# Performance work log

Hardware: AMD Instinct MI355X
Metric: run time of the kernel (lower is better)

The kernel has to match this reference:

```python
import jax, jax.numpy as jnp
import numpy as np

WS = 7       # window size per spatial dim
SHIFT = 3    # cyclic shift = WS // 2
HEADS = 6


def _rel_pos_index():
    # [N, N] index into the (2*WS-1)^3 relative-position-bias table
    c = np.stack(np.meshgrid(np.arange(WS), np.arange(WS), np.arange(WS), indexing='ij')).reshape(3, -1)
    rel = (c[:, :, None] - c[:, None, :]).transpose(1, 2, 0) + (WS - 1)
    rel[:, :, 0] *= (2 * WS - 1) ** 2
    rel[:, :, 1] *= (2 * WS - 1)
    return rel.sum(-1)


def _attn_mask(D, H, W):
    # shifted-window attention mask: [nW, N, N] with 0 / -100
    img = np.zeros((D, H, W))
    sl = (slice(0, -WS), slice(-WS, -SHIFT), slice(-SHIFT, None))
    cnt = 0
    for d in sl:
        for h in sl:
            for w in sl:
                img[d, h, w] = cnt
                cnt += 1
    m = img.reshape(D // WS, WS, H // WS, WS, W // WS, WS).transpose(0, 2, 4, 1, 3, 5).reshape(-1, WS ** 3)
    return np.where(m[:, None, :] != m[:, :, None], -100.0, 0.0).astype(np.float32)


def _ln(x, g, b):
    mu = x.mean(-1, keepdims=True)
    var = ((x - mu) ** 2).mean(-1, keepdims=True)
    return (x - mu) * jax.lax.rsqrt(var + 1e-5) * g + b


def _win_part(x):
    B, D, H, W, C = x.shape
    x = x.reshape(B, D // WS, WS, H // WS, WS, W // WS, WS, C)
    return x.transpose(0, 1, 3, 5, 2, 4, 6, 7).reshape(B, -1, WS ** 3, C)


def _win_rev(xw, D, H, W):
    B, _, _, C = xw.shape
    x = xw.reshape(B, D // WS, H // WS, W // WS, WS, WS, WS, C)
    return x.transpose(0, 1, 4, 2, 5, 3, 6, 7).reshape(B, D, H, W, C)


def setup_inputs() -> dict:
    key = jax.random.key(0)
    ks = jax.random.split(key, 8)
    C, dff, Nh = 192, 768, HEADS
    s = 0.02
    return {
        'x': jax.random.normal(ks[0], (2, 28, 28, 28, C), jnp.float32),
        'ln1_g': jnp.ones((C,), jnp.float32),
        'ln1_b': jnp.zeros((C,), jnp.float32),
        'qkv_w': jax.random.normal(ks[1], (3 * C, C), jnp.float32) * s,
        'qkv_b': jnp.zeros((3 * C,), jnp.float32),
        'rpb': jax.random.normal(ks[2], ((2 * WS - 1) ** 3, Nh), jnp.float32) * s,
        'proj_w': jax.random.normal(ks[3], (C, C), jnp.float32) * s,
        'proj_b': jnp.zeros((C,), jnp.float32),
        'ln2_g': jnp.ones((C,), jnp.float32),
        'ln2_b': jnp.zeros((C,), jnp.float32),
        'fc1_w': jax.random.normal(ks[4], (dff, C), jnp.float32) * s,
        'fc1_b': jnp.zeros((dff,), jnp.float32),
        'fc2_w': jax.random.normal(ks[5], (C, dff), jnp.float32) * s,
        'fc2_b': jnp.zeros((C,), jnp.float32),
    }


def reference(x, ln1_g, ln1_b, qkv_w, qkv_b, rpb, proj_w, proj_b, ln2_g, ln2_b, fc1_w, fc1_b, fc2_w, fc2_b):
    B, D, H, W, C = x.shape
    hd = C // HEADS
    N = WS ** 3
    idx = jnp.asarray(_rel_pos_index())          # [N, N] int
    mask = jnp.asarray(_attn_mask(D, H, W))      # [nW, N, N]

    shortcut = x
    h = _ln(x, ln1_g, ln1_b)
    h = jnp.roll(h, (-SHIFT, -SHIFT, -SHIFT), axis=(1, 2, 3))
    xw = _win_part(h)                            # [B, nW, N, C]
    nW = xw.shape[1]

    qkv = xw @ qkv_w.T + qkv_b                   # [B, nW, N, 3C]
    qkv = qkv.reshape(B, nW, N, 3, HEADS, hd).transpose(3, 0, 1, 4, 2, 5)  # [3,B,nW,h,N,hd]
    q, k, v = qkv[0], qkv[1], qkv[2]

    scale = hd ** -0.5
    attn = jnp.einsum('bwhnd,bwhmd->bwhnm', q * scale, k)  # [B,nW,h,N,N]
    bias = rpb[idx].transpose(2, 0, 1)           # [h, N, N]
    attn = attn + bias + mask[None, :, None]
    attn = jax.nn.softmax(attn, axis=-1)

    o = jnp.einsum('bwhnm,bwhmd->bwhnd', attn, v)
    o = o.transpose(0, 1, 3, 2, 4).reshape(B, nW, N, C)
    o = o @ proj_w.T + proj_b
    o = _win_rev(o, D, H, W)
    o = jnp.roll(o, (SHIFT, SHIFT, SHIFT), axis=(1, 2, 3))

    x = shortcut + o
    h2 = _ln(x, ln2_g, ln2_b)
    h2 = jax.nn.gelu(h2 @ fc1_w.T + fc1_b, approximate=False)
    return x + (h2 @ fc2_w.T + fc2_b)
```

## Files before the change

kernel.cpp:

```cpp
#include <hip/hip_runtime.h>
#include <hip/hip_bf16.h>
#include <math.h>

typedef __hip_bfloat16 bf16;
typedef unsigned short u16;
typedef __attribute__((ext_vector_type(8))) short bf16x8;
typedef __attribute__((ext_vector_type(4))) float f32x4;
typedef __attribute__((ext_vector_type(16))) float f32x16;
typedef __attribute__((ext_vector_type(4))) unsigned u32x4;

__device__ __forceinline__ float us2f(u16 u) { return __uint_as_float(((unsigned)u) << 16); }
__device__ __forceinline__ u16 f2us(float f) { bf16 h = __float2bfloat16(f); return *(u16*)&h; }

__device__ __forceinline__ float wave_bcast_sum(float v) {
#pragma unroll
    for (int off = 32; off > 0; off >>= 1) v += __shfl_down(v, off);
    return __shfl(v, 0);
}

__device__ __forceinline__ void glds16(const u16* g, u16* l) {
    __builtin_amdgcn_global_load_lds((const __attribute__((address_space(1))) void*)g,
                                     (__attribute__((address_space(3))) void*)l, 16, 0, 0);
}

__global__ __launch_bounds__(256) void k_prep(
    const float* __restrict__ qkv_w, const float* __restrict__ proj_w,
    const float* __restrict__ rpb,
    u16* __restrict__ qkv_wb, u16* __restrict__ proj_wb, float* __restrict__ biasF)
{
    int idx = blockIdx.x * 256 + threadIdx.x;
    if (idx < 110592) { qkv_wb[idx] = f2us(qkv_w[idx]); return; }
    idx -= 110592;
    if (idx < 36864) { proj_wb[idx] = f2us(proj_w[idx]); return; }
    idx -= 36864;
    if (idx >= 6 * 11 * 11 * 1024) return;
    int r16 = idx & 15;
    int lane = (idx >> 4) & 63;
    int cell = idx >> 10;
    int chunk = cell % 11;
    int t2 = cell / 11;
    int tile = t2 % 11;
    int h = t2 / 11;
    int g = r16 >> 2, q = r16 & 3;
    int hi = lane >> 5, l31 = lane & 31;
    int n = tile * 32 + l31;
    int m = chunk * 32 + 4 * hi + 8 * g + q;
    float v = 0.0f;
    if (m < 343 && n < 343) {
        int ni = n / 49, nr = n - ni * 49, nj = nr / 7, nk = nr - nj * 7;
        int mi = m / 49, mr = m - mi * 49, mj = mr / 7, mk = mr - mj * 7;
        int d = (ni - mi) * 169 + (nj - mj) * 13 + (nk - mk) + 1098;
        v = rpb[d * 6 + h] * 5.656854249492381f;
    }
    biasF[idx] = v;
}

__global__ __launch_bounds__(256) void k_f2b2(
    const float* __restrict__ fc1_w, const float* __restrict__ fc2_w,
    u16* __restrict__ fc1_wb, u16* __restrict__ fc2_wb)
{
    int idx = blockIdx.x * 256 + threadIdx.x;
    if (idx < 147456) fc1_wb[idx] = f2us(fc1_w[idx]);
    else fc2_wb[idx - 147456] = f2us(fc2_w[idx - 147456]);
}

__global__ __launch_bounds__(256) void k_ln1_winpart(
    const float* __restrict__ x, const float* __restrict__ g, const float* __restrict__ b,
    u16* __restrict__ out)
{
    int lane = threadIdx.x & 63;
    int t = blockIdx.x * 4 + (threadIdx.x >> 6);
    int bidx = t / (64 * 343);
    int r = t - bidx * (64 * 343);
    int w = r / 343;
    int n = r - w * 343;
    int wd = w >> 4, wh = (w >> 2) & 3, ww = w & 3;
    int i = n / 49, rem = n - i * 49;
    int j = rem / 7, k = rem - j * 7;
    int sd = wd * 7 + i + 3; if (sd >= 28) sd -= 28;
    int sh = wh * 7 + j + 3; if (sh >= 28) sh -= 28;
    int sw = ww * 7 + k + 3; if (sw >= 28) sw -= 28;
    size_t src = ((((size_t)bidx * 28 + sd) * 28 + sh) * 28 + sw) * 192;
    float v0 = x[src + lane], v1 = x[src + lane + 64], v2 = x[src + lane + 128];
    float s  = wave_bcast_sum(v0 + v1 + v2);
    float mu = s * (1.0f / 192.0f);
    float s2 = wave_bcast_sum(v0 * v0 + v1 * v1 + v2 * v2);
    float rs = rsqrtf(s2 * (1.0f / 192.0f) - mu * mu + 1e-5f);
    u16* op = out + (size_t)t * 192;
    op[lane]       = f2us((v0 - mu) * rs * g[lane]       + b[lane]);
    op[lane + 64]  = f2us((v1 - mu) * rs * g[lane + 64]  + b[lane + 64]);
    op[lane + 128] = f2us((v2 - mu) * rs * g[lane + 128] + b[lane + 128]);
}

__global__ __launch_bounds__(256) void k_add_winrev_ln2(
    const float* __restrict__ x, const u16* __restrict__ projw,
    const float* __restrict__ g, const float* __restrict__ b,
    float* __restrict__ x1, u16* __restrict__ h2)
{
    int lane = threadIdx.x & 63;
    int t = blockIdx.x * 4 + (threadIdx.x >> 6);
    int sw_ = t % 28, t1 = t / 28;
    int sh_ = t1 % 28, t2 = t1 / 28;
    int sd_ = t2 % 28, bidx = t2 / 28;
    int rd = sd_ + 25; if (rd >= 28) rd -= 28;
    int rh = sh_ + 25; if (rh >= 28) rh -= 28;
    int rw = sw_ + 25; if (rw >= 28) rw -= 28;
    int wd = rd / 7, i = rd - wd * 7;
    int wh = rh / 7, j = rh - wh * 7;
    int ww = rw / 7, k = rw - ww * 7;
    int w = (wd << 4) + (wh << 2) + ww;
    int n = (i * 7 + j) * 7 + k;
    size_t src = (((size_t)(bidx * 64 + w)) * 343 + n) * 192;
    const float* xp = x + (size_t)t * 192;
    float v0 = xp[lane]       + us2f(projw[src + lane]);
    float v1 = xp[lane + 64]  + us2f(projw[src + lane + 64]);
    float v2 = xp[lane + 128] + us2f(projw[src + lane + 128]);
    float* op = x1 + (size_t)t * 192;
    op[lane] = v0; op[lane + 64] = v1; op[lane + 128] = v2;
    float s  = wave_bcast_sum(v0 + v1 + v2);
    float mu = s * (1.0f / 192.0f);
    float s2 = wave_bcast_sum(v0 * v0 + v1 * v1 + v2 * v2);
    float rs = rsqrtf(s2 * (1.0f / 192.0f) - mu * mu + 1e-5f);
    u16* hp = h2 + (size_t)t * 192;
    hp[lane]       = f2us((v0 - mu) * rs * g[lane]       + b[lane]);
    hp[lane + 64]  = f2us((v1 - mu) * rs * g[lane + 64]  + b[lane + 64]);
    hp[lane + 128] = f2us((v2 - mu) * rs * g[lane + 128] + b[lane + 128]);
}

template<int ACT, int OUT, int GX>
__global__ __launch_bounds__(256) void k_gemm_mfma(
    const u16* __restrict__ A, const u16* __restrict__ W, const float* __restrict__ bias,
    u16* __restrict__ outB, float* __restrict__ outF, const float* __restrict__ resid,
    int M, int Nc, int K)
{
    __shared__ __align__(16) u16 As[2][128 * 64];
    __shared__ __align__(16) u16 Bs[2][64 * 64];
    int tid = threadIdx.x;
    int lane = tid & 63, wv = tid >> 6;
    int quad = lane >> 4, l16 = lane & 15;

    int nwg = gridDim.x, orig = blockIdx.x;
    int q = nwg >> 3, r = nwg & 7;
    int xcd = orig & 7, lin = orig >> 3;
    int L = (xcd < r ? xcd * (q + 1) : r * (q + 1) + (xcd - r) * q) + lin;
    int bx = L % GX, by = L / GX;
    int m0 = by << 7, n0 = bx << 6;

    f32x4 acc[2][4] = {};

    int srow = wv * 8 + (lane >> 3);
    int swz  = ((lane & 7) << 3) ^ (((lane >> 3) & 7) << 3);
    const u16* gA = A + (size_t)(m0 + srow) * K + swz;
    const u16* gB = W + (size_t)(n0 + srow) * K + swz;
    int rsA = 32 * K;

    int nst = K >> 6;
#define STAGE(buf, k0)                                                        \
    {                                                                         \
        _Pragma("unroll")                                                     \
        for (int i = 0; i < 4; i++)                                           \
            glds16(gA + (size_t)i * rsA + (k0), &As[buf][(i * 4 + wv) * 512]); \
        _Pragma("unroll")                                                     \
        for (int i = 0; i < 2; i++)                                           \
            glds16(gB + (size_t)i * rsA + (k0), &Bs[buf][(i * 4 + wv) * 512]); \
    }

    STAGE(0, 0);
    asm volatile("s_waitcnt vmcnt(0)" ::: "memory");
    __builtin_amdgcn_s_barrier();

    int rswz = (l16 & 7) << 3;
    int cur = 0;
    for (int t = 0; t < nst; ++t) {
        if (t + 1 < nst) STAGE(cur ^ 1, (t + 1) << 6);
#pragma unroll
        for (int kk = 0; kk < 2; kk++) {
            int ko = (kk * 32 + quad * 8) ^ rswz;
            bf16x8 af[2], bfr[4];
#pragma unroll
            for (int mt = 0; mt < 2; mt++)
                af[mt] = *(const bf16x8*)&As[cur][(wv * 32 + mt * 16 + l16) * 64 + ko];
#pragma unroll
            for (int nt = 0; nt < 4; nt++)
                bfr[nt] = *(const bf16x8*)&Bs[cur][(nt * 16 + l16) * 64 + ko];
#pragma unroll
            for (int mt = 0; mt < 2; mt++)
#pragma unroll
                for (int nt = 0; nt < 4; nt++)
                    acc[mt][nt] = __builtin_amdgcn_mfma_f32_16x16x32_bf16(af[mt], bfr[nt], acc[mt][nt], 0, 0, 0);
        }
        asm volatile("s_waitcnt vmcnt(0)" ::: "memory");
        __builtin_amdgcn_s_barrier();
        cur ^= 1;
    }
#undef STAGE
#pragma unroll
    for (int mt = 0; mt < 2; mt++) {
#pragma unroll
        for (int nt = 0; nt < 4; nt++) {
#pragma unroll
            for (int r2 = 0; r2 < 4; r2++) {
                int m = m0 + wv * 32 + mt * 16 + quad * 4 + r2;
                int n = n0 + nt * 16 + l16;
                float v = acc[mt][nt][r2] + bias[n];
                if (ACT == 1) v = 0.5f * v * (1.0f + erff(v * 0.70710678118654752f));
                size_t off = (size_t)m * Nc + n;
                if (OUT == 1) outB[off] = f2us(v);
                else outF[off] = resid[off] + v;
            }
        }
    }
}

__global__ __launch_bounds__(704, 6) void k_attn(
    const u16* __restrict__ qkv, const float* __restrict__ biasF, u16* __restrict__ o_win)
{
    int head = blockIdx.x;
    int w = blockIdx.y;
    int bidx = blockIdx.z;
    __shared__ __align__(16) u16 Ks[352 * 40];
    __shared__ __align__(16) u16 Vt[32 * 360];
    __shared__ unsigned char lab[352];
    int tid = threadIdx.x;
    int lane = tid & 63, wv = tid >> 6;
    int hi = lane >> 5, l31 = lane & 31;
    size_t base = ((size_t)(bidx * 64 + w)) * 343;

    for (int i = tid; i < 2816; i += 704) {
        int m = i >> 3;
        int d4 = (i & 7) << 2;
        ushort4 kv = {0, 0, 0, 0}, vv = {0, 0, 0, 0};
        if (m < 343) {
            size_t off = (base + m) * 576 + head * 32 + d4;
            kv = *(const ushort4*)(qkv + off + 192);
            vv = *(const ushort4*)(qkv + off + 384);
        }
        *(ushort4*)&Ks[m * 40 + d4] = kv;
        Vt[(d4 + 0) * 360 + m] = vv.x;
        Vt[(d4 + 1) * 360 + m] = vv.y;
        Vt[(d4 + 2) * 360 + m] = vv.z;
        Vt[(d4 + 3) * 360 + m] = vv.w;
    }
    int wd = w >> 4, wh = (w >> 2) & 3, ww = w & 3;
    bool uni = (wd < 3) && (wh < 3) && (ww < 3);
    for (int n = tid; n < 352; n += 704) {
        unsigned char lv = 255;
        if (n < 343) {
            int i = n / 49, rem = n - i * 49;
            int j = rem / 7, k = rem - j * 7;
            int gd = wd * 7 + i, gh = wh * 7 + j, gw = ww * 7 + k;
            int ld_ = (gd < 21) ? 0 : ((gd < 25) ? 1 : 2);
            int lh_ = (gh < 21) ? 0 : ((gh < 25) ? 1 : 2);
            int lw_ = (gw < 21) ? 0 : ((gw < 25) ? 1 : 2);
            lv = (unsigned char)(ld_ * 9 + lh_ * 3 + lw_);
        }
        lab[n] = lv;
    }
    __syncthreads();

    const float SCALE = 0.17677669529663687f;
    const f32x16 z16 = {0,0,0,0,0,0,0,0,0,0,0,0,0,0,0,0};

    int tile = wv;
    int n0 = tile * 32;
    int nq = n0 + l31; if (nq > 342) nq = 342;
    const u16* qp = qkv + (base + nq) * 576 + head * 32;
    bf16x8 bq0 = *(const bf16x8*)(qp + hi * 8);
    bf16x8 bq1 = *(const bf16x8*)(qp + 16 + hi * 8);
    unsigned lr = lab[n0 + l31];
    const float* bfr = biasF + ((size_t)(head * 11 + tile) * 11) * 1024 + lane * 16;

    f32x16 o = z16;
    float psum = 0.0f;

    auto chunk = [&](int c, int mode) {
        int mb = c * 32;
        const u16* kp = &Ks[(mb + l31) * 40 + hi * 8];
        bf16x8 ka0 = *(const bf16x8*)kp;
        bf16x8 ka1 = *(const bf16x8*)(kp + 16);
        f32x16 s;
        const float* bc = bfr + c * 1024;
#pragma unroll
        for (int g = 0; g < 4; ++g)
            ((float4*)&s)[g] = *(const float4*)(bc + g * 4);
        s = __builtin_amdgcn_mfma_f32_32x32x16_bf16(ka0, bq0, s, 0, 0, 0);
        s = __builtin_amdgcn_mfma_f32_32x32x16_bf16(ka1, bq1, s, 0, 0, 0);
        float p[16];
        if (mode == 0) {
#pragma unroll
            for (int r = 0; r < 16; ++r) p[r] = __expf(s[r] * SCALE);
        } else if (mode == 1) {
#pragma unroll
            for (int r = 0; r < 16; ++r) {
                int m = mb + 4 * hi + 8 * (r >> 2) + (r & 3);
                float e = __expf(s[r] * SCALE);
                p[r] = (m < 343) ? e : 0.0f;
            }
        } else {
            unsigned labw[4];
#pragma unroll
            for (int g = 0; g < 4; ++g)
                labw[g] = *(const unsigned*)&lab[mb + hi * 4 + g * 8];
#pragma unroll
            for (int r = 0; r < 16; ++r) {
                float e = __expf(s[r] * SCALE);
                p[r] = (((labw[r >> 2] >> (8 * (r & 3))) & 255u) == lr) ? e : 0.0f;
            }
        }
#pragma unroll
        for (int r = 0; r < 16; ++r) psum += p[r];
        unsigned pk0, pk1, pk2, pk3, pk4, pk5, pk6, pk7;
        asm("v_cvt_pk_bf16_f32 %0, %1, %2" : "=v"(pk0) : "v"(p[0]),  "v"(p[1]));
        asm("v_cvt_pk_bf16_f32 %0, %1, %2" : "=v"(pk1) : "v"(p[2]),  "v"(p[3]));
        asm("v_cvt_pk_bf16_f32 %0, %1, %2" : "=v"(pk2) : "v"(p[4]),  "v"(p[5]));
        asm("v_cvt_pk_bf16_f32 %0, %1, %2" : "=v"(pk3) : "v"(p[6]),  "v"(p[7]));
        asm("v_cvt_pk_bf16_f32 %0, %1, %2" : "=v"(pk4) : "v"(p[8]),  "v"(p[9]));
        asm("v_cvt_pk_bf16_f32 %0, %1, %2" : "=v"(pk5) : "v"(p[10]), "v"(p[11]));
        asm("v_cvt_pk_bf16_f32 %0, %1, %2" : "=v"(pk6) : "v"(p[12]), "v"(p[13]));
        asm("v_cvt_pk_bf16_f32 %0, %1, %2" : "=v"(pk7) : "v"(p[14]), "v"(p[15]));
        asm volatile("v_permlane32_swap_b32 %0, %1" : "+v"(pk0), "+v"(pk2));
        asm volatile("v_permlane32_swap_b32 %0, %1" : "+v"(pk1), "+v"(pk3));
        asm volatile("v_permlane32_swap_b32 %0, %1" : "+v"(pk4), "+v"(pk6));
        asm volatile("v_permlane32_swap_b32 %0, %1" : "+v"(pk5), "+v"(pk7));
        u32x4 A1 = {pk0, pk1, pk2, pk3};
        u32x4 A2 = {pk4, pk5, pk6, pk7};
        bf16x8 pa0 = __builtin_bit_cast(bf16x8, A1);
        bf16x8 pa1 = __builtin_bit_cast(bf16x8, A2);
        const u16* vp = &Vt[l31 * 360 + mb + hi * 8];
        bf16x8 vb0 = *(const bf16x8*)vp;
        bf16x8 vb1 = *(const bf16x8*)(vp + 16);
        o = __builtin_amdgcn_mfma_f32_32x32x16_bf16(pa0, vb0, o, 0, 0, 0);
        o = __builtin_amdgcn_mfma_f32_32x32x16_bf16(pa1, vb1, o, 0, 0, 0);
    };

    if (uni) {
#pragma unroll 2
        for (int c = 0; c < 10; ++c) chunk(c, 0);
        chunk(10, 1);
    } else {
#pragma unroll 2
        for (int c = 0; c < 11; ++c) chunk(c, 2);
    }

    psum += __shfl_xor(psum, 32);
    float inv = 1.0f / psum;
#pragma unroll
    for (int r = 0; r < 16; ++r) {
        int crow = (r & 3) + 8 * (r >> 2) + 4 * hi;
        int n = n0 + crow;
        float invc = __shfl(inv, crow);
        if (n < 343) {
            u16* op = o_win + (base + n) * 192 + head * 32;
            op[l31] = f2us(o[r] * invc);
        }
    }
}

extern "C" void kernel_launch(void* const* d_in, const int* in_sizes, int n_in,
                              void* d_out, int out_size, void* d_ws, size_t ws_size,
                              hipStream_t stream)
{
    const float* x      = (const float*)d_in[0];
    const float* ln1_g  = (const float*)d_in[1];
    const float* ln1_b  = (const float*)d_in[2];
    const float* qkv_w  = (const float*)d_in[3];
    const float* qkv_b  = (const float*)d_in[4];
    const float* rpb    = (const float*)d_in[5];
    const float* proj_w = (const float*)d_in[6];
    const float* proj_b = (const float*)d_in[7];
    const float* ln2_g  = (const float*)d_in[8];
    const float* ln2_b  = (const float*)d_in[9];
    const float* fc1_w  = (const float*)d_in[10];
    const float* fc1_b  = (const float*)d_in[11];
    const float* fc2_w  = (const float*)d_in[12];
    const float* fc2_b  = (const float*)d_in[13];

    const int M = 43904;
    const size_t MC  = (size_t)M * 192;
    const size_t MC2 = MC * 2;

    char* ws = (char*)d_ws;
    u16* hA     = (u16*)ws;
    u16* qkvb   = (u16*)(ws + MC2);
    u16* projw  = (u16*)(ws + MC2);
    u16* gbuf   = (u16*)(ws + MC2);
    u16* fc1_wb = (u16*)(ws + 51u * 1024 * 1024);
    u16* fc2_wb = (u16*)(ws + 51u * 1024 * 1024 + 294912);
    float* out  = (float*)d_out;
    u16* qkv_wb  = (u16*)d_out;
    u16* proj_wb = (u16*)d_out + 110592;
    float* biasF = (float*)((char*)d_out + 4u * 1024 * 1024);

    k_prep<<<3481, 256, 0, stream>>>(qkv_w, proj_w, rpb, qkv_wb, proj_wb, biasF);
    k_ln1_winpart<<<M / 4, 256, 0, stream>>>(x, ln1_g, ln1_b, hA);
    k_gemm_mfma<0, 1, 9><<<3087, 256, 0, stream>>>(hA, qkv_wb, qkv_b, qkvb, nullptr, nullptr, M, 576, 192);
    k_attn<<<dim3(6, 64, 2), 704, 0, stream>>>(qkvb, biasF, hA);
    k_f2b2<<<1152, 256, 0, stream>>>(fc1_w, fc2_w, fc1_wb, fc2_wb);
    k_gemm_mfma<0, 1, 3><<<1029, 256, 0, stream>>>(hA, proj_wb, proj_b, projw, nullptr, nullptr, M, 192, 192);
    k_add_winrev_ln2<<<M / 4, 256, 0, stream>>>(x, projw, ln2_g, ln2_b, out, hA);
    const int CH0 = 22016, CH1 = 21888;
    k_gemm_mfma<1, 1, 12><<<2064, 256, 0, stream>>>(hA, fc1_wb, fc1_b, gbuf, nullptr, nullptr, CH0, 768, 192);
    k_gemm_mfma<0, 2, 3><<<516, 256, 0, stream>>>(gbuf, fc2_wb, fc2_b, nullptr, out, out, CH0, 192, 768);
    k_gemm_mfma<1, 1, 12><<<2052, 256, 0, stream>>>(hA + (size_t)CH0 * 192, fc1_wb, fc1_b, gbuf, nullptr, nullptr, CH1, 768, 192);
    k_gemm_mfma<0, 2, 3><<<513, 256, 0, stream>>>(gbuf, fc2_wb, fc2_b, nullptr, out + (size_t)CH0 * 192, out + (size_t)CH0 * 192, CH1, 192, 768);
}
```

Measured before the change: 286.2 us.

## Fuse MLP fc1+GELU+fc2 into one kernel keeping hidden activations in LDS

Replaces the four chunked GEMM launches for the MLP (fc1 with GELU writing a bf16 hidden buffer to global, then fc2 reading it back) with a single fused kernel. Each 512-thread block loads a 64-row tile of the normalized input into LDS, computes the 768-wide hidden layer in two 384-column halves, applies GELU into LDS, and accumulates fc2 directly before adding the residual. This removes the global round trip of the large hidden tensor and cuts launches. In exchange, weights are read straight from global/L2 with no LDS staging, each block has only 686 blocks of parallelism, and register and LDS pressure (about 75 KB of LDS) may limit occupancy.

```diff
diff --git a/kernel.cpp b/kernel.cpp
--- a/kernel.cpp
+++ b/kernel.cpp
@@ -212,6 +212,86 @@
     }
 }
 
+__global__ __launch_bounds__(512, 4) void k_mlp(
+    const u16* __restrict__ hA, const u16* __restrict__ w1, const float* __restrict__ b1,
+    const u16* __restrict__ w2, const float* __restrict__ b2, float* __restrict__ out)
+{
+    __shared__ __align__(16) u16 Asm[64 * 200];
+    __shared__ __align__(16) u16 Hs[64 * 392];
+    int tid = threadIdx.x;
+    int lane = tid & 63, wv = tid >> 6;
+    int quad = lane >> 4, l16 = lane & 15;
+    int m0 = blockIdx.x * 64;
+
+    for (int i = tid; i < 3072; i += 512) {
+        int row = i / 48, c4 = (i - row * 48) * 4;
+        *(ushort4*)&Asm[row * 200 + c4] = *(const ushort4*)(hA + (size_t)(m0 + row) * 192 + c4);
+    }
+    __syncthreads();
+
+    f32x4 accB[6] = {};
+    int mB = wv & 3;
+    int nB0 = (wv >> 2) * 96;
+    int hc0 = wv * 48;
+
+#pragma unroll
+    for (int h = 0; h < 2; ++h) {
+        f32x4 accA[4][3] = {};
+#pragma unroll
+        for (int kk = 0; kk < 6; ++kk) {
+            bf16x8 af[4];
+#pragma unroll
+            for (int m = 0; m < 4; m++)
+                af[m] = *(const bf16x8*)&Asm[(m * 16 + l16) * 200 + kk * 32 + quad * 8];
+#pragma unroll
+            for (int nt = 0; nt < 3; nt++) {
+                int hrow = h * 384 + hc0 + nt * 16 + l16;
+                bf16x8 wf = *(const bf16x8*)(w1 + (size_t)hrow * 192 + kk * 32 + quad * 8);
+#pragma unroll
+                for (int m = 0; m < 4; m++)
+                    accA[m][nt] = __builtin_amdgcn_mfma_f32_16x16x32_bf16(af[m], wf, accA[m][nt], 0, 0, 0);
+            }
+        }
+        if (h == 1) __syncthreads();
+#pragma unroll
+        for (int nt = 0; nt < 3; nt++) {
+            int col = hc0 + nt * 16 + l16;
+            float bb = b1[h * 384 + col];
+#pragma unroll
+            for (int m = 0; m < 4; m++) {
+#pragma unroll
+                for (int r = 0; r < 4; r++) {
+                    float v = accA[m][nt][r] + bb;
+                    float g = 0.5f * v * (1.0f + erff(v * 0.70710678118654752f));
+                    Hs[(m * 16 + quad * 4 + r) * 392 + col] = f2us(g);
+                }
+            }
+        }
+        __syncthreads();
+#pragma unroll
+        for (int kk = 0; kk < 12; ++kk) {
+            bf16x8 hf = *(const bf16x8*)&Hs[(mB * 16 + l16) * 392 + kk * 32 + quad * 8];
+#pragma unroll
+            for (int nt = 0; nt < 6; nt++) {
+                int orow = nB0 + nt * 16 + l16;
+                bf16x8 w2f = *(const bf16x8*)(w2 + (size_t)orow * 768 + h * 384 + kk * 32 + quad * 8);
+                accB[nt] = __builtin_amdgcn_mfma_f32_16x16x32_bf16(hf, w2f, accB[nt], 0, 0, 0);
+            }
+        }
+    }
+#pragma unroll
+    for (int nt = 0; nt < 6; nt++) {
+        int n = nB0 + nt * 16 + l16;
+        float bb = b2[n];
+#pragma unroll
+        for (int r = 0; r < 4; r++) {
+            int m = m0 + mB * 16 + quad * 4 + r;
+            size_t off = (size_t)m * 192 + n;
+            out[off] = out[off] + accB[nt][r] + bb;
+        }
+    }
+}
+
 __global__ __launch_bounds__(704, 6) void k_attn(
     const u16* __restrict__ qkv, const float* __restrict__ biasF, u16* __restrict__ o_win)
 {
@@ -383,7 +463,6 @@
     u16* hA     = (u16*)ws;
     u16* qkvb   = (u16*)(ws + MC2);
     u16* projw  = (u16*)(ws + MC2);
-    u16* gbuf   = (u16*)(ws + MC2);
     u16* fc1_wb = (u16*)(ws + 51u * 1024 * 1024);
     u16* fc2_wb = (u16*)(ws + 51u * 1024 * 1024 + 294912);
     float* out  = (float*)d_out;
@@ -398,9 +477,5 @@
     k_f2b2<<<1152, 256, 0, stream>>>(fc1_w, fc2_w, fc1_wb, fc2_wb);
     k_gemm_mfma<0, 1, 3><<<1029, 256, 0, stream>>>(hA, proj_wb, proj_b, projw, nullptr, nullptr, M, 192, 192);
     k_add_winrev_ln2<<<M / 4, 256, 0, stream>>>(x, projw, ln2_g, ln2_b, out, hA);
-    const int CH0 = 22016, CH1 = 21888;
-    k_gemm_mfma<1, 1, 12><<<2064, 256, 0, stream>>>(hA, fc1_wb, fc1_b, gbuf, nullptr, nullptr, CH0, 768, 192);
-    k_gemm_mfma<0, 2, 3><<<516, 256, 0, stream>>>(gbuf, fc2_wb, fc2_b, nullptr, out, out, CH0, 192, 768);
-    k_gemm_mfma<1, 1, 12><<<2052, 256, 0, stream>>>(hA + (size_t)CH0 * 192, fc1_wb, fc1_b, gbuf, nullptr, nullptr, CH1, 768, 192);
-    k_gemm_mfma<0, 2, 3><<<513, 256, 0, stream>>>(gbuf, fc2_wb, fc2_b, nullptr, out + (size_t)CH0 * 192, out + (size_t)CH0 * 192, CH1, 192, 768);
-}
+    k_mlp<<<686, 512, 0, stream>>>(hA, fc1_wb, fc1_b, fc2_wb, fc2_b, out);
+}
```

Measured after the change: 355.9 us. 24.3% more time.
